# Kernel tuning notes

Hardware: AMD Instinct MI355X
Metric: run time of the kernel (lower is better)

## Reference

```python
import jax, jax.numpy as jnp
import numpy as np

N_SRC = 100000
N_DST = 50000
N_EDGES = 1600000
D_IN = 128
D_OUT = 64


def setup_inputs() -> dict:
    key = jax.random.key(0)
    ks = jax.random.split(key, 6)
    x = jax.random.normal(ks[0], (N_SRC, D_IN), dtype=jnp.float32)
    W_l = jax.random.normal(ks[1], (D_IN, D_OUT), dtype=jnp.float32) * (1.0 / np.sqrt(D_IN))
    b_l = jax.random.normal(ks[2], (D_OUT,), dtype=jnp.float32) * 0.01
    W_r = jax.random.normal(ks[3], (D_IN, D_OUT), dtype=jnp.float32) * (1.0 / np.sqrt(D_IN))
    src = jax.random.randint(ks[4], (N_EDGES,), 0, N_SRC, dtype=jnp.int64)
    dst = jax.random.randint(ks[5], (N_EDGES,), 0, N_DST, dtype=jnp.int64)
    edge_index = jnp.stack([src, dst], axis=0)
    return {"x": x, "W_l": W_l, "b_l": b_l, "W_r": W_r,
            "edge_index": edge_index, "n_dst": N_DST}


def reference(x, W_l, b_l, W_r, edge_index, n_dst):
    src, dst = edge_index[0], edge_index[1]
    # gather source features along edges: [E, D_in]
    msgs = x[src]
    # mean aggregation at destination nodes
    agg = jax.ops.segment_sum(msgs, dst, num_segments=n_dst)          # [n_dst, D_in]
    cnt = jax.ops.segment_sum(jnp.ones_like(dst, dtype=x.dtype), dst,
                              num_segments=n_dst)                     # [n_dst]
    mean = agg / jnp.maximum(cnt, 1.0)[:, None]
    x_target = x[:n_dst]
    # SAGEConv: lin_l(mean_agg) + lin_r(x_target)
    out = mean @ W_l + b_l + x_target @ W_r                           # [n_dst, D_out]
    return jax.nn.log_softmax(out, axis=-1)
```

## Files before the change

kernel.cpp:

```cpp
#include <hip/hip_runtime.h>
#include <math.h>

#define DIN  128
#define DOUT 64
#define PROWS 64
#define XPITCH 132
#define BSH  6
#define BMSK 63
#define BCAP 2496

__device__ inline unsigned short f2bf(float f) {
    unsigned u = __float_as_uint(f);
    u += 0x7fffu + ((u >> 16) & 1u);
    return (unsigned short)(u >> 16);
}
__device__ inline float bflo(unsigned u) { return __uint_as_float(u << 16); }
__device__ inline float bfhi(unsigned u) { return __uint_as_float(u & 0xffff0000u); }

__global__ void __launch_bounds__(256) build_k(
    const int* __restrict__ ei, unsigned* __restrict__ gTail,
    int* __restrict__ bucketBuf,
    const float* __restrict__ x, const float* __restrict__ Wl,
    const float* __restrict__ bl, const float* __restrict__ Wr,
    unsigned short* __restrict__ y, float* __restrict__ zout,
    int E, int nFill, int P, int nyb, int n_src, int n_dst, int nB)
{
    __shared__ float s_x[PROWS * XPITCH];
    const int b = blockIdx.x;
    const int fq = b / P;
    const bool isFill = ((b % P) == 0) && (fq < nFill);

    if (isFill) {
        int* s_i  = (int*)s_x;
        int* lcnt = s_i;
        int* lpos = s_i + 1024;
        int* s_gb = s_i + 2048;
        const int t = threadIdx.x;
        const int myb = (fq * 256 + t) * 8;
        const bool full = (myb + 8 <= E);
        const bool any  = (myb < E);
        int4 sa, sb4, da, db;
        if (full) {
            sa  = *(const int4*)(ei + myb);
            sb4 = *(const int4*)(ei + myb + 4);
            da  = *(const int4*)(ei + E + myb);
            db  = *(const int4*)(ei + E + myb + 4);
        }
        lcnt[t] = 0; lcnt[t + 256] = 0; lcnt[t + 512] = 0; lcnt[t + 768] = 0;
        lpos[t] = 0; lpos[t + 256] = 0; lpos[t + 512] = 0; lpos[t + 768] = 0;
        __syncthreads();
        if (full) {
            atomicAdd(&lcnt[da.x >> BSH], 1); atomicAdd(&lcnt[da.y >> BSH], 1);
            atomicAdd(&lcnt[da.z >> BSH], 1); atomicAdd(&lcnt[da.w >> BSH], 1);
            atomicAdd(&lcnt[db.x >> BSH], 1); atomicAdd(&lcnt[db.y >> BSH], 1);
            atomicAdd(&lcnt[db.z >> BSH], 1); atomicAdd(&lcnt[db.w >> BSH], 1);
        } else if (any) {
            for (int i = myb; i < E && i < myb + 8; ++i)
                atomicAdd(&lcnt[ei[E + i] >> BSH], 1);
        }
        __syncthreads();
        for (int bk = t; bk < nB; bk += 256)
            s_gb[bk] = (int)atomicAdd(&gTail[bk], (unsigned)lcnt[bk]);
        __syncthreads();
#define PLACE(S, D) { int bk = (D) >> BSH; int p = atomicAdd(&lpos[bk], 1);          \
                      unsigned pos = (unsigned)(s_gb[bk] + p);                        \
                      if (pos < BCAP) bucketBuf[(size_t)bk * BCAP + pos] =            \
                          ((S) << BSH) | ((D) & BMSK); }
        if (full) {
            PLACE(sa.x,  da.x) PLACE(sa.y,  da.y) PLACE(sa.z,  da.z) PLACE(sa.w,  da.w)
            PLACE(sb4.x, db.x) PLACE(sb4.y, db.y) PLACE(sb4.z, db.z) PLACE(sb4.w, db.w)
        } else if (any) {
            for (int i = myb; i < E && i < myb + 8; ++i) {
                int s = ei[i], d = ei[E + i];
                PLACE(s, d)
            }
        }
#undef PLACE
        return;
    }

    const int fillsBefore = (fq + 1 < nFill) ? (fq + 1) : nFill;
    const int pb = b - fillsBefore;
    const int t  = threadIdx.x;
    const bool isY = (pb < nyb);
    const int rowBase = (isY ? pb : pb - nyb) * PROWS;
    const int nRows = isY ? n_src : n_dst;
    const float* __restrict__ W = isY ? Wl : Wr;

    {
        const float* xsrc = x + (size_t)rowBase * DIN;
        #pragma unroll
        for (int j = 0; j < 8; ++j) {
            int fi  = t + 256 * j;
            int row = fi >> 5, c4 = fi & 31;
            if (rowBase + row < nRows) {
                float4 v = *(const float4*)(xsrc + (size_t)fi * 4);
                *(float4*)(&s_x[row * XPITCH + c4 * 4]) = v;
            }
        }
    }
    __syncthreads();

    const int cg = t & 15;
    const int rg = t >> 4;
    const int r0 = rg * 4;
    const float* wp = W + cg * 4;

    float4 acc0 = {0.f,0.f,0.f,0.f};
    float4 acc1 = {0.f,0.f,0.f,0.f};
    float4 acc2 = {0.f,0.f,0.f,0.f};
    float4 acc3 = {0.f,0.f,0.f,0.f};

#define ROWFMA(acc, xv)                                                                     \
    acc.x = fmaf(xv.w, w3.x, fmaf(xv.z, w2.x, fmaf(xv.y, w1.x, fmaf(xv.x, w0.x, acc.x)))); \
    acc.y = fmaf(xv.w, w3.y, fmaf(xv.z, w2.y, fmaf(xv.y, w1.y, fmaf(xv.x, w0.y, acc.y)))); \
    acc.z = fmaf(xv.w, w3.z, fmaf(xv.z, w2.z, fmaf(xv.y, w1.z, fmaf(xv.x, w0.z, acc.z)))); \
    acc.w = fmaf(xv.w, w3.w, fmaf(xv.z, w2.w, fmaf(xv.y, w1.w, fmaf(xv.x, w0.w, acc.w))));

    #pragma unroll 2
    for (int k = 0; k < DIN; k += 4) {
        float4 w0 = *(const float4*)(wp + (size_t)(k + 0) * DOUT);
        float4 w1 = *(const float4*)(wp + (size_t)(k + 1) * DOUT);
        float4 w2 = *(const float4*)(wp + (size_t)(k + 2) * DOUT);
        float4 w3 = *(const float4*)(wp + (size_t)(k + 3) * DOUT);
        float4 x0 = *(const float4*)(&s_x[(r0 + 0) * XPITCH + k]);
        float4 x1 = *(const float4*)(&s_x[(r0 + 1) * XPITCH + k]);
        float4 x2 = *(const float4*)(&s_x[(r0 + 2) * XPITCH + k]);
        float4 x3 = *(const float4*)(&s_x[(r0 + 3) * XPITCH + k]);
        ROWFMA(acc0, x0)
        ROWFMA(acc1, x1)
        ROWFMA(acc2, x2)
        ROWFMA(acc3, x3)
    }
#undef ROWFMA

    if (isY) {
        float4 av[4] = {acc0, acc1, acc2, acc3};
        #pragma unroll
        for (int r = 0; r < 4; ++r) {
            int row = rowBase + r0 + r;
            if (row < nRows) {
                uint2 pk;
                pk.x = (unsigned)f2bf(av[r].x) | ((unsigned)f2bf(av[r].y) << 16);
                pk.y = (unsigned)f2bf(av[r].z) | ((unsigned)f2bf(av[r].w) << 16);
                *(uint2*)(y + (size_t)row * DOUT + cg * 4) = pk;
            }
        }
    } else {
        const float4 bv = *(const float4*)(bl + cg * 4);
        float4 av[4] = {acc0, acc1, acc2, acc3};
        #pragma unroll
        for (int r = 0; r < 4; ++r) {
            int row = rowBase + r0 + r;
            if (row < nRows) {
                float4 o;
                o.x = av[r].x + bv.x; o.y = av[r].y + bv.y;
                o.z = av[r].z + bv.z; o.w = av[r].w + bv.w;
                *(float4*)(zout + (size_t)row * DOUT + cg * 4) = o;
            }
        }
    }
}

__global__ void __launch_bounds__(512) bg_k(
    const unsigned* __restrict__ gTail, const int* __restrict__ bucketBuf,
    const unsigned short* __restrict__ y,
    float* __restrict__ out, int n_dst)
{
    __shared__ int s_ent[BCAP];
    __shared__ int s_csr[BCAP];
    __shared__ int s_hist[64];
    __shared__ int s_ofs[64];
    __shared__ int s_start[65];
    const int b = blockIdx.x, t = threadIdx.x;
    const int lane = t & 63, wave = t >> 6;

    if (t < 64) s_hist[t] = 0;
    int m = (int)gTail[b]; if (m > BCAP) m = BCAP;
    __syncthreads();

    const int* bb = bucketBuf + (size_t)b * BCAP;
    const int4* bb4 = (const int4*)bb;
    int4* se4 = (int4*)s_ent;
    const int m4 = m >> 2;
    for (int i4 = t; i4 < m4; i4 += 512) {
        int4 e4 = bb4[i4];
        se4[i4] = e4;
        atomicAdd(&s_hist[e4.x & BMSK], 1);
        atomicAdd(&s_hist[e4.y & BMSK], 1);
        atomicAdd(&s_hist[e4.z & BMSK], 1);
        atomicAdd(&s_hist[e4.w & BMSK], 1);
    }
    for (int i = (m4 << 2) + t; i < m; i += 512) {
        int e = bb[i];
        s_ent[i] = e;
        atomicAdd(&s_hist[e & BMSK], 1);
    }
    __syncthreads();

    if (wave == 0) {
        int h = s_hist[lane];
        int v = h;
        for (int o = 1; o < 64; o <<= 1) {
            int u = __shfl_up(v, o);
            if (lane >= o) v += u;
        }
        s_start[lane + 1] = v;
        if (lane == 0) s_start[0] = 0;
        s_ofs[lane] = v - h;
    }
    __syncthreads();

    for (int i4 = t; i4 < m4; i4 += 512) {
        int4 e4 = se4[i4];
        int p0 = atomicAdd(&s_ofs[e4.x & BMSK], 1); s_csr[p0] = e4.x >> BSH;
        int p1 = atomicAdd(&s_ofs[e4.y & BMSK], 1); s_csr[p1] = e4.y >> BSH;
        int p2 = atomicAdd(&s_ofs[e4.z & BMSK], 1); s_csr[p2] = e4.z >> BSH;
        int p3 = atomicAdd(&s_ofs[e4.w & BMSK], 1); s_csr[p3] = e4.w >> BSH;
    }
    for (int i = (m4 << 2) + t; i < m; i += 512) {
        int e = s_ent[i];
        int p = atomicAdd(&s_ofs[e & BMSK], 1);
        s_csr[p] = e >> BSH;
    }
    __syncthreads();

    const int dbase = b << BSH;
    int nloc = n_dst - dbase; if (nloc > 64) nloc = 64;
    const int g  = lane >> 3;
    const int c8 = lane & 7;
    const uint4* yw = (const uint4*)y;

#define ACC8(al, ah, u)                                              \
    al.x += bflo(u.x); al.y += bfhi(u.x);                            \
    al.z += bflo(u.y); al.w += bfhi(u.y);                            \
    ah.x += bflo(u.z); ah.y += bfhi(u.z);                            \
    ah.z += bflo(u.w); ah.w += bfhi(u.w);

    for (int r = wave; r < nloc; r += 8) {
        const int row = dbase + r;
        const int start = s_start[r];
        const int deg = s_start[r + 1] - start;

        const float4 zv0 = *(const float4*)(out + (size_t)row * DOUT + c8 * 8);
        const float4 zv1 = *(const float4*)(out + (size_t)row * DOUT + c8 * 8 + 4);

        float4 a0l = {0,0,0,0}, a0h = {0,0,0,0};
        float4 a1l = {0,0,0,0}, a1h = {0,0,0,0};
        float4 a2l = {0,0,0,0}, a2h = {0,0,0,0};
        float4 a3l = {0,0,0,0}, a3h = {0,0,0,0};

        for (int co = 0; co < deg; co += 64) {
            int rem = deg - co; if (rem > 64) rem = 64;
            int idx = (lane < rem) ? s_csr[start + co + lane] : 0;
            int i = 0;
            for (; i + 32 <= rem; i += 32) {
                int s0 = __shfl(idx, i + g);
                int s1 = __shfl(idx, i + 8 + g);
                int s2 = __shfl(idx, i + 16 + g);
                int s3 = __shfl(idx, i + 24 + g);
                uint4 u0 = yw[(size_t)s0 * 8 + c8];
                uint4 u1 = yw[(size_t)s1 * 8 + c8];
                uint4 u2 = yw[(size_t)s2 * 8 + c8];
                uint4 u3 = yw[(size_t)s3 * 8 + c8];
                ACC8(a0l, a0h, u0)
                ACC8(a1l, a1h, u1)
                ACC8(a2l, a2h, u2)
                ACC8(a3l, a3h, u3)
            }
            for (; i < rem; i += 8) {
                int e = i + g;
                int s0 = __shfl(idx, e);
                if (e < rem) {
                    uint4 u = yw[(size_t)s0 * 8 + c8];
                    ACC8(a0l, a0h, u)
                }
            }
        }

        float4 sl, sh;
        sl.x = (a0l.x + a1l.x) + (a2l.x + a3l.x);
        sl.y = (a0l.y + a1l.y) + (a2l.y + a3l.y);
        sl.z = (a0l.z + a1l.z) + (a2l.z + a3l.z);
        sl.w = (a0l.w + a1l.w) + (a2l.w + a3l.w);
        sh.x = (a0h.x + a1h.x) + (a2h.x + a3h.x);
        sh.y = (a0h.y + a1h.y) + (a2h.y + a3h.y);
        sh.z = (a0h.z + a1h.z) + (a2h.z + a3h.z);
        sh.w = (a0h.w + a1h.w) + (a2h.w + a3h.w);

        #pragma unroll
        for (int o = 32; o >= 8; o >>= 1) {
            sl.x += __shfl_xor(sl.x, o); sl.y += __shfl_xor(sl.y, o);
            sl.z += __shfl_xor(sl.z, o); sl.w += __shfl_xor(sl.w, o);
            sh.x += __shfl_xor(sh.x, o); sh.y += __shfl_xor(sh.y, o);
            sh.z += __shfl_xor(sh.z, o); sh.w += __shfl_xor(sh.w, o);
        }

        const float scale = 1.0f / (float)(deg > 0 ? deg : 1);
        float4 v0, v1;
        v0.x = sl.x * scale + zv0.x; v0.y = sl.y * scale + zv0.y;
        v0.z = sl.z * scale + zv0.z; v0.w = sl.w * scale + zv0.w;
        v1.x = sh.x * scale + zv1.x; v1.y = sh.y * scale + zv1.y;
        v1.z = sh.z * scale + zv1.z; v1.w = sh.w * scale + zv1.w;

        float mx = fmaxf(fmaxf(fmaxf(v0.x, v0.y), fmaxf(v0.z, v0.w)),
                         fmaxf(fmaxf(v1.x, v1.y), fmaxf(v1.z, v1.w)));
        for (int o = 4; o >= 1; o >>= 1) mx = fmaxf(mx, __shfl_xor(mx, o));
        float s = expf(v0.x - mx) + expf(v0.y - mx) + expf(v0.z - mx) + expf(v0.w - mx)
                + expf(v1.x - mx) + expf(v1.y - mx) + expf(v1.z - mx) + expf(v1.w - mx);
        for (int o = 4; o >= 1; o >>= 1) s += __shfl_xor(s, o);
        const float lse = mx + logf(s);

        if (lane < 8) {
            float4 o0, o1;
            o0.x = v0.x - lse; o0.y = v0.y - lse; o0.z = v0.z - lse; o0.w = v0.w - lse;
            o1.x = v1.x - lse; o1.y = v1.y - lse; o1.z = v1.z - lse; o1.w = v1.w - lse;
            *(float4*)(out + (size_t)row * DOUT + c8 * 8)     = o0;
            *(float4*)(out + (size_t)row * DOUT + c8 * 8 + 4) = o1;
        }
    }
#undef ACC8
}

extern "C" void kernel_launch(void* const* d_in, const int* in_sizes, int n_in,
                              void* d_out, int out_size, void* d_ws, size_t ws_size,
                              hipStream_t stream)
{
    const float* x  = (const float*)d_in[0];
    const float* Wl = (const float*)d_in[1];
    const float* bl = (const float*)d_in[2];
    const float* Wr = (const float*)d_in[3];
    const int*   ei = (const int*)d_in[4];

    const int E     = in_sizes[4] / 2;
    const int n_src = in_sizes[0] / DIN;
    const int n_dst = out_size / DOUT;
    const int nB    = (n_dst + (1 << BSH) - 1) >> BSH;

    unsigned* gTail = (unsigned*)d_ws;
    int* bucketBuf = (int*)d_ws + 1024;
    unsigned short* yb = (unsigned short*)(bucketBuf + (size_t)nB * BCAP);

    hipMemsetAsync(gTail, 0, 1024 * sizeof(unsigned), stream);

    int nFill = (E + 2047) / 2048;
    int nyb = (n_src + PROWS - 1) / PROWS;
    int nzb = (n_dst + PROWS - 1) / PROWS;
    int total = nFill + nyb + nzb;
    int P = (total + nFill - 1) / nFill;

    build_k<<<total, 256, 0, stream>>>(
        ei, gTail, bucketBuf, x, Wl, bl, Wr, yb, (float*)d_out,
        E, nFill, P, nyb, n_src, n_dst, nB);

    bg_k<<<nB, 512, 0, stream>>>(gTail, bucketBuf, yb, (float*)d_out, n_dst);
}
```

Before: 209.4 us.

## Tile projection GEMM over K with shared-memory staging of W and x

Splits the 128-wide K dimension into 32-wide chunks. For each chunk, a slice of x and the matching slice of W are staged in shared memory before the FMA loop runs. Previously W was read straight from global memory by every thread. The change cuts LDS footprint per block, which may raise occupancy, and replaces global/L2 W reads with LDS reads. The cost is four times as many barriers and no overlap between loads and compute.

```diff
diff --git a/kernel.cpp b/kernel.cpp
--- a/kernel.cpp
+++ b/kernel.cpp
@@ -4,7 +4,8 @@
 #define DIN  128
 #define DOUT 64
 #define PROWS 64
-#define XPITCH 132
+#define KS   32
+#define XSP  36
 #define BSH  6
 #define BMSK 63
 #define BCAP 2496
@@ -25,13 +26,13 @@
     unsigned short* __restrict__ y, float* __restrict__ zout,
     int E, int nFill, int P, int nyb, int n_src, int n_dst, int nB)
 {
-    __shared__ float s_x[PROWS * XPITCH];
+    __shared__ float s_mem[PROWS * XSP + KS * DOUT];
     const int b = blockIdx.x;
     const int fq = b / P;
     const bool isFill = ((b % P) == 0) && (fq < nFill);
 
     if (isFill) {
-        int* s_i  = (int*)s_x;
+        int* s_i  = (int*)s_mem;
         int* lcnt = s_i;
         int* lpos = s_i + 1024;
         int* s_gb = s_i + 2048;
@@ -87,24 +88,12 @@
     const int nRows = isY ? n_src : n_dst;
     const float* __restrict__ W = isY ? Wl : Wr;
 
-    {
-        const float* xsrc = x + (size_t)rowBase * DIN;
-        #pragma unroll
-        for (int j = 0; j < 8; ++j) {
-            int fi  = t + 256 * j;
-            int row = fi >> 5, c4 = fi & 31;
-            if (rowBase + row < nRows) {
-                float4 v = *(const float4*)(xsrc + (size_t)fi * 4);
-                *(float4*)(&s_x[row * XPITCH + c4 * 4]) = v;
-            }
-        }
-    }
-    __syncthreads();
+    float* s_xs = s_mem;
+    float* s_ws = s_mem + PROWS * XSP;
 
     const int cg = t & 15;
     const int rg = t >> 4;
     const int r0 = rg * 4;
-    const float* wp = W + cg * 4;
 
     float4 acc0 = {0.f,0.f,0.f,0.f};
     float4 acc1 = {0.f,0.f,0.f,0.f};
@@ -117,20 +106,46 @@
     acc.z = fmaf(xv.w, w3.z, fmaf(xv.z, w2.z, fmaf(xv.y, w1.z, fmaf(xv.x, w0.z, acc.z)))); \
     acc.w = fmaf(xv.w, w3.w, fmaf(xv.z, w2.w, fmaf(xv.y, w1.w, fmaf(xv.x, w0.w, acc.w))));
 
-    #pragma unroll 2
-    for (int k = 0; k < DIN; k += 4) {
-        float4 w0 = *(const float4*)(wp + (size_t)(k + 0) * DOUT);
-        float4 w1 = *(const float4*)(wp + (size_t)(k + 1) * DOUT);
-        float4 w2 = *(const float4*)(wp + (size_t)(k + 2) * DOUT);
-        float4 w3 = *(const float4*)(wp + (size_t)(k + 3) * DOUT);
-        float4 x0 = *(const float4*)(&s_x[(r0 + 0) * XPITCH + k]);
-        float4 x1 = *(const float4*)(&s_x[(r0 + 1) * XPITCH + k]);
-        float4 x2 = *(const float4*)(&s_x[(r0 + 2) * XPITCH + k]);
-        float4 x3 = *(const float4*)(&s_x[(r0 + 3) * XPITCH + k]);
-        ROWFMA(acc0, x0)
-        ROWFMA(acc1, x1)
-        ROWFMA(acc2, x2)
-        ROWFMA(acc3, x3)
+    for (int k0 = 0; k0 < DIN; k0 += KS) {
+        {
+            const float* xs = x + (size_t)rowBase * DIN + k0;
+            #pragma unroll
+            for (int j = 0; j < 2; ++j) {
+                int fi = t + 256 * j;
+                int row = fi >> 3, c4 = fi & 7;
+                if (rowBase + row < nRows) {
+                    float4 v = *(const float4*)(xs + (size_t)row * DIN + c4 * 4);
+                    *(float4*)(&s_xs[row * XSP + c4 * 4]) = v;
+                }
+            }
+            const float* ws = W + (size_t)k0 * DOUT;
+            #pragma unroll
+            for (int j = 0; j < 2; ++j) {
+                int fi = t + 256 * j;
+                int row = fi >> 4, c4 = fi & 15;
+                float4 v = *(const float4*)(ws + row * DOUT + c4 * 4);
+                *(float4*)(&s_ws[row * DOUT + c4 * 4]) = v;
+            }
+        }
+        __syncthreads();
+
+        const float* wp = s_ws + cg * 4;
+        #pragma unroll 2
+        for (int k = 0; k < KS; k += 4) {
+            float4 w0 = *(const float4*)(wp + (k + 0) * DOUT);
+            float4 w1 = *(const float4*)(wp + (k + 1) * DOUT);
+            float4 w2 = *(const float4*)(wp + (k + 2) * DOUT);
+            float4 w3 = *(const float4*)(wp + (k + 3) * DOUT);
+            float4 x0 = *(const float4*)(&s_xs[(r0 + 0) * XSP + k]);
+            float4 x1 = *(const float4*)(&s_xs[(r0 + 1) * XSP + k]);
+            float4 x2 = *(const float4*)(&s_xs[(r0 + 2) * XSP + k]);
+            float4 x3 = *(const float4*)(&s_xs[(r0 + 3) * XSP + k]);
+            ROWFMA(acc0, x0)
+            ROWFMA(acc1, x1)
+            ROWFMA(acc2, x2)
+            ROWFMA(acc3, x3)
+        }
+        __syncthreads();
     }
 #undef ROWFMA
 
```

Result: faster. 200.5 us (-4.2%).
